# Performance work log

Hardware: AMD Instinct MI355X
Metric: run time of the kernel (lower is better)

Reference implementation:

```python
import jax, jax.numpy as jnp
import numpy as np

EPSILON = 1e-05


def _sq_dist(x, e):
    # x: [N, D], e: [M, D] -> [N, M] squared euclidean distances (addmm form)
    return (jnp.sum(e ** 2, axis=1)[None, :]
            + jnp.sum(x ** 2, axis=1, keepdims=True)
            - 2.0 * (x @ e.T))


def _mode_along_last(idx, M):
    # idx: [B, T] int32 -> [B] mode (smallest value among most frequent, like torch.mode)
    def one(row):
        counts = jnp.zeros((M,), dtype=jnp.int32).at[row].add(1)
        return jnp.argmax(counts)
    return jax.vmap(one)(idx)


def setup_inputs() -> dict:
    key = jax.random.key(0)
    k1, k2, k3 = jax.random.split(key, 3)
    B, T, D, M = 64, 512, 512, 1024
    audio_semantic = jax.random.normal(k1, (B, T, D), dtype=jnp.float32)
    video_semantic = jax.random.normal(k2, (B, T, D), dtype=jnp.float32)
    init_bound = 1.0 / M
    embedding = jax.random.uniform(k3, (M, 2 * D), dtype=jnp.float32,
                                   minval=-init_bound, maxval=init_bound)
    log_ratio = float(np.log(0.8 / 0.2))
    modality_weights = jnp.zeros((M, 4), dtype=jnp.float32)
    modality_weights = modality_weights.at[:, 0].set(log_ratio).at[:, 3].set(log_ratio)
    return {"audio_semantic": audio_semantic, "video_semantic": video_semantic,
            "embedding": embedding, "modality_weights": modality_weights, "epoch": 1}


def reference(audio_semantic, video_semantic, embedding, modality_weights, epoch):
    M, D_total = embedding.shape
    B, T, D = audio_semantic.shape
    video_embedding = embedding[:, :D]   # [M, D]
    audio_embedding = embedding[:, D:]   # [M, D]

    a_flat = audio_semantic.reshape(-1, D)  # [B*T, D]
    v_flat = video_semantic.reshape(-1, D)

    v_distances = _sq_dist(v_flat, video_embedding)  # [B*T, M]
    a_distances = _sq_dist(a_flat, audio_embedding)

    # cross-modal matching probabilities (clamp for sqrt numerical safety)
    v_ph = jax.nn.softmax(-jnp.sqrt(jnp.maximum(v_distances, 0.0)), axis=1)
    a_ph = jax.nn.softmax(-jnp.sqrt(jnp.maximum(a_distances, 0.0)), axis=1)
    v_pH = jnp.mean(v_ph.reshape(B, T, M), axis=1)  # [B, M]
    a_pH = jnp.mean(a_ph.reshape(B, T, M), axis=1)

    Scode = a_pH @ jnp.log(v_pH.T + 1e-10) + v_pH @ jnp.log(a_pH.T + 1e-10)  # [B, B]
    MaxScode = jnp.max(-Scode)
    EScode = jnp.exp(Scode + MaxScode)
    EScode_sumdim1 = jnp.sum(EScode, axis=1)
    Lcmcm_av = -jnp.mean(jnp.log(jnp.diag(EScode) / (EScode_sumdim1 + EPSILON)))

    v_indices = jnp.argmin(v_distances, axis=-1)  # [B*T]
    a_indices = jnp.argmin(a_distances, axis=-1)

    # straight-through quantization
    v_q = video_embedding[v_indices].reshape(B, T, D)
    a_q = audio_embedding[a_indices].reshape(B, T, D)
    v_quantized = video_semantic + jax.lax.stop_gradient(v_q - video_semantic)
    a_quantized = audio_semantic + jax.lax.stop_gradient(a_q - audio_semantic)

    v_full_vectors = embedding[v_indices].reshape(B, T, D_total)
    a_full_vectors = embedding[a_indices].reshape(B, T, D_total)

    v_mode = _mode_along_last(v_indices.reshape(B, T), M)
    a_mode = _mode_along_last(a_indices.reshape(B, T), M)
    equal_num = jnp.sum(v_mode == a_mode)

    return (v_full_vectors, a_full_vectors, v_quantized, a_quantized, Lcmcm_av, equal_num)
```

## Files before the change

### kernel.cpp

```cpp
#include <hip/hip_runtime.h>
#include <stdint.h>

typedef unsigned long long u64;

#define NROWS 32768
#define DK    512
#define MM    1024

#define WS_ET    0u
#define WS_SE    4194304u
#define WS_PH    4202496u
#define WS_CNT   4726784u
#define WS_IDX   5251072u
#define WS_SC    5513216u
#define WS_MODES 5529600u

__global__ void k_se(const float* __restrict__ E, float* __restrict__ se) {
  int t = threadIdx.x;
  int row = blockIdx.x * 4 + (t >> 6);
  int lane = t & 63;
  int mod = row >> 10, m = row & 1023;
  const float4* er = (const float4*)(E + (size_t)m * 1024 + mod * 512);
  float4 a = er[lane * 2], b = er[lane * 2 + 1];
  float s = a.x*a.x + a.y*a.y + a.z*a.z + a.w*a.w
          + b.x*b.x + b.y*b.y + b.z*b.z + b.w*b.w;
  #pragma unroll
  for (int o = 1; o < 64; o <<= 1) s += __shfl_xor(s, o, 64);
  if (lane == 0) se[row] = s;
}

__global__ void k_transpose(const float* __restrict__ E, float* __restrict__ Et) {
  __shared__ float tile[32][33];
  int t = threadIdx.x;
  int kt = blockIdx.x & 15, mt = blockIdx.x >> 4, mod = blockIdx.y;
  int j = t & 31, i0 = t >> 5;
  for (int ii = i0; ii < 32; ii += 8)
    tile[ii][j] = E[(size_t)(mt*32 + ii) * 1024 + mod*512 + kt*32 + j];
  __syncthreads();
  int mm2 = t & 31, kx = t >> 5;
  for (int kk = kx; kk < 32; kk += 8)
    Et[(size_t)mod * 524288 + (size_t)(kt*32 + kk) * 1024 + mt*32 + mm2] = tile[mm2][kk];
}

__global__ __launch_bounds__(256, 2) void k_main(
    const float* __restrict__ vsem, const float* __restrict__ asem,
    const float* __restrict__ Et, const float* __restrict__ se,
    float* __restrict__ pH, int* __restrict__ cnt, int* __restrict__ idx)
{
  __shared__ float Bs[16][1024];
  __shared__ __align__(16) float As[16][36];
  __shared__ float pH_part[1024];
  __shared__ float sx_lds[32];

  const int t = threadIdx.x;
  const int mod = blockIdx.y;
  const int r0 = blockIdx.x * 32;
  const int rg = t >> 6, cg = t & 63;
  const float* x = mod ? asem : vsem;

  {
    int r = t >> 4, kl = t & 15;
    #pragma unroll
    for (int h = 0; h < 2; ++h) {
      const float* xr = x + (size_t)(r0 + r + h * 16) * DK;
      float s = 0.f;
      for (int k = kl; k < DK; k += 16) { float v = xr[k]; s = fmaf(v, v, s); }
      #pragma unroll
      for (int o = 1; o < 16; o <<= 1) s += __shfl_xor(s, o, 64);
      if (kl == 0) sx_lds[r + h * 16] = s;
    }
  }

  float acc[128];
  #pragma unroll
  for (int q = 0; q < 128; ++q) acc[q] = 0.f;

  for (int k0 = 0; k0 < DK; k0 += 16) {
    __syncthreads();
    {
      int akl = t & 15, ar = t >> 4;
      As[akl][ar]      = x[(size_t)(r0 + ar) * DK + k0 + akl];
      As[akl][ar + 16] = x[(size_t)(r0 + ar + 16) * DK + k0 + akl];
    }
    #pragma unroll
    for (int kk = 0; kk < 16; ++kk)
      *(float4*)&Bs[kk][t * 4] =
          ((const float4*)(Et + (size_t)mod * 524288 + (size_t)(k0 + kk) * 1024))[t];
    __syncthreads();
    #pragma unroll
    for (int kk = 0; kk < 16; ++kk) {
      const float4 a0 = *(const float4*)&As[kk][rg * 8];
      const float4 a1 = *(const float4*)&As[kk][rg * 8 + 4];
      const float4 b0 = *(const float4*)&Bs[kk][cg * 4];
      const float4 b1 = *(const float4*)&Bs[kk][256 + cg * 4];
      const float4 b2 = *(const float4*)&Bs[kk][512 + cg * 4];
      const float4 b3 = *(const float4*)&Bs[kk][768 + cg * 4];
      #pragma unroll
      for (int rr = 0; rr < 8; ++rr) {
        const float av = rr == 0 ? a0.x : rr == 1 ? a0.y : rr == 2 ? a0.z :
                         rr == 3 ? a0.w : rr == 4 ? a1.x : rr == 5 ? a1.y :
                         rr == 6 ? a1.z : a1.w;
        float* ar = acc + rr * 16;
        ar[0] = fmaf(av, b0.x, ar[0]);  ar[1] = fmaf(av, b0.y, ar[1]);
        ar[2] = fmaf(av, b0.z, ar[2]);  ar[3] = fmaf(av, b0.w, ar[3]);
        ar[4] = fmaf(av, b1.x, ar[4]);  ar[5] = fmaf(av, b1.y, ar[5]);
        ar[6] = fmaf(av, b1.z, ar[6]);  ar[7] = fmaf(av, b1.w, ar[7]);
        ar[8] = fmaf(av, b2.x, ar[8]);  ar[9] = fmaf(av, b2.y, ar[9]);
        ar[10] = fmaf(av, b2.z, ar[10]); ar[11] = fmaf(av, b2.w, ar[11]);
        ar[12] = fmaf(av, b3.x, ar[12]); ar[13] = fmaf(av, b3.y, ar[13]);
        ar[14] = fmaf(av, b3.z, ar[14]); ar[15] = fmaf(av, b3.w, ar[15]);
      }
    }
  }

  float sxv[8];
  #pragma unroll
  for (int rr = 0; rr < 8; ++rr) sxv[rr] = sx_lds[rg * 8 + rr];
  const float* seB = se + mod * 1024;

  float rowsum[8] = {0.f, 0.f, 0.f, 0.f, 0.f, 0.f, 0.f, 0.f};
  u64 bk[8] = {~0ull, ~0ull, ~0ull, ~0ull, ~0ull, ~0ull, ~0ull, ~0ull};
  #pragma unroll
  for (int j = 0; j < 4; ++j)
    #pragma unroll
    for (int i = 0; i < 4; ++i) {
      const int m = j * 256 + cg * 4 + i;
      const float sem = seB[m];
      #pragma unroll
      for (int rr = 0; rr < 8; ++rr) {
        const float d = (sem + sxv[rr]) - 2.0f * acc[rr * 16 + j * 4 + i];
        const float s = sqrtf(fmaxf(d, 0.0f));
        const float ww = __expf(-s);
        acc[rr * 16 + j * 4 + i] = ww;
        rowsum[rr] += ww;
        unsigned ub = __float_as_uint(d);
        ub = (ub & 0x80000000u) ? ~ub : (ub | 0x80000000u);
        u64 key = ((u64)ub << 32) | (u64)(unsigned)m;
        bk[rr] = key < bk[rr] ? key : bk[rr];
      }
    }
  #pragma unroll
  for (int o = 1; o < 64; o <<= 1) {
    #pragma unroll
    for (int rr = 0; rr < 8; ++rr) {
      rowsum[rr] += __shfl_xor(rowsum[rr], o, 64);
      u64 ok = __shfl_xor(bk[rr], o, 64);
      bk[rr] = ok < bk[rr] ? ok : bk[rr];
    }
  }

  const int b = r0 >> 9;
  if (cg == 0) {
    #pragma unroll
    for (int rr = 0; rr < 8; ++rr) {
      const int row = r0 + rg * 8 + rr;
      const int m = (int)(bk[rr] & 0xFFFFFFFFull);
      idx[mod * NROWS + row] = m;
      atomicAdd(&cnt[((mod * 64 + b) << 10) + m], 1);
    }
  }

  float inv[8];
  #pragma unroll
  for (int rr = 0; rr < 8; ++rr) inv[rr] = 1.0f / rowsum[rr];

  for (int q = t; q < 1024; q += 256) pH_part[q] = 0.f;
  __syncthreads();
  #pragma unroll
  for (int j = 0; j < 4; ++j)
    #pragma unroll
    for (int i = 0; i < 4; ++i) {
      const int m = j * 256 + cg * 4 + i;
      float v = 0.f;
      #pragma unroll
      for (int rr = 0; rr < 8; ++rr) v += acc[rr * 16 + j * 4 + i] * inv[rr];
      atomicAdd(&pH_part[m], v);
    }
  __syncthreads();
  for (int q = t; q < 1024; q += 256)
    atomicAdd(&pH[((mod * 64 + b) << 10) + q], pH_part[q] * (1.0f / 512.0f));
}

__global__ void k_modes(const int* __restrict__ cnt, int* __restrict__ modes) {
  __shared__ u64 red[4];
  int t = threadIdx.x;
  int mod = blockIdx.x >> 6, b = blockIdx.x & 63;
  const int* c = cnt + ((mod * 64 + b) << 10);
  u64 best = 0;
  for (int m = t; m < 1024; m += 256) {
    u64 key = ((u64)(unsigned)c[m] << 32) | (u64)(0xFFFFFFFFu - (unsigned)m);
    best = key > best ? key : best;
  }
  #pragma unroll
  for (int o = 1; o < 64; o <<= 1) { u64 ok = __shfl_xor(best, o, 64); best = ok > best ? ok : best; }
  if ((t & 63) == 0) red[t >> 6] = best;
  __syncthreads();
  if (t == 0) {
    #pragma unroll
    for (int q = 1; q < 4; ++q) best = red[q] > best ? red[q] : best;
    modes[mod * 64 + b] = (int)(0xFFFFFFFFu - (unsigned)(best & 0xFFFFFFFFull));
  }
}

__global__ void k_equal(const int* __restrict__ modes, float* __restrict__ out5) {
  int t = threadIdx.x;
  float e = (modes[t] == modes[64 + t]) ? 1.0f : 0.0f;
  #pragma unroll
  for (int o = 1; o < 64; o <<= 1) e += __shfl_xor(e, o, 64);
  if (t == 0) out5[0] = e;
}

__global__ void k_scode(const float* __restrict__ pH, float* __restrict__ Sc) {
  int t = threadIdx.x;
  int i = blockIdx.x;
  int j = t >> 2, part = t & 3;
  const float* vH = pH;
  const float* aH = pH + 65536;
  const float* ai = aH + i * 1024;
  const float* vi = vH + i * 1024;
  const float* vj = vH + j * 1024;
  const float* aj = aH + j * 1024;
  float s = 0.f;
  for (int m = part * 256; m < part * 256 + 256; ++m)
    s += ai[m] * logf(vj[m] + 1e-10f) + vi[m] * logf(aj[m] + 1e-10f);
  s += __shfl_xor(s, 1, 64);
  s += __shfl_xor(s, 2, 64);
  if (part == 0) Sc[i * 64 + j] = s;
}

__global__ void k_lcmcm(const float* __restrict__ Sc, float* __restrict__ out4) {
  __shared__ float red[4];
  __shared__ float maxs_sh;
  int t = threadIdx.x;
  float mx = -3.402823466e38f;
  for (int q = t; q < 4096; q += 256) mx = fmaxf(mx, -Sc[q]);
  #pragma unroll
  for (int o = 1; o < 64; o <<= 1) mx = fmaxf(mx, __shfl_xor(mx, o, 64));
  if ((t & 63) == 0) red[t >> 6] = mx;
  __syncthreads();
  if (t == 0) maxs_sh = fmaxf(fmaxf(red[0], red[1]), fmaxf(red[2], red[3]));
  __syncthreads();
  float maxS = maxs_sh;
  if (t < 64) {
    float sum = 0.f, diag = 0.f;
    for (int j2 = 0; j2 < 64; ++j2) {
      float e = expf(Sc[t * 64 + j2] + maxS);
      sum += e;
      if (j2 == t) diag = e;
    }
    float li = logf(diag / (sum + 1e-5f));
    #pragma unroll
    for (int o = 1; o < 64; o <<= 1) li += __shfl_xor(li, o, 64);
    if (t == 0) out4[0] = -(li * (1.0f / 64.0f));
  }
}

__global__ __launch_bounds__(256) void k_gather(
    const float* __restrict__ E, const float* __restrict__ vsem,
    const float* __restrict__ asem, const int* __restrict__ idx,
    float* __restrict__ out0, float* __restrict__ out1,
    float* __restrict__ out2, float* __restrict__ out3)
{
  int n = blockIdx.x, t = threadIdx.x;
  int iv = idx[n], ia = idx[NROWS + n];
  const float4* E4 = (const float4*)E;
  ((float4*)(out0 + (size_t)n * 1024))[t] = E4[iv * 256 + t];
  ((float4*)(out1 + (size_t)n * 1024))[t] = E4[ia * 256 + t];
  if (t < 128) {
    float4 q = E4[iv * 256 + t];
    float4 xv = ((const float4*)(vsem + (size_t)n * 512))[t];
    float4 r;
    r.x = xv.x + (q.x - xv.x); r.y = xv.y + (q.y - xv.y);
    r.z = xv.z + (q.z - xv.z); r.w = xv.w + (q.w - xv.w);
    ((float4*)(out2 + (size_t)n * 512))[t] = r;
  } else {
    int u = t - 128;
    float4 q = E4[ia * 256 + 128 + u];
    float4 xa = ((const float4*)(asem + (size_t)n * 512))[u];
    float4 r;
    r.x = xa.x + (q.x - xa.x); r.y = xa.y + (q.y - xa.y);
    r.z = xa.z + (q.z - xa.z); r.w = xa.w + (q.w - xa.w);
    ((float4*)(out3 + (size_t)n * 512))[u] = r;
  }
}

extern "C" void kernel_launch(void* const* d_in, const int* in_sizes, int n_in,
                              void* d_out, int out_size, void* d_ws, size_t ws_size,
                              hipStream_t stream) {
  const float* asem = (const float*)d_in[0];
  const float* vsem = (const float*)d_in[1];
  const float* E    = (const float*)d_in[2];
  char* ws = (char*)d_ws;
  float* Et    = (float*)(ws + WS_ET);
  float* se    = (float*)(ws + WS_SE);
  float* pH    = (float*)(ws + WS_PH);
  int*   cnt   = (int*)(ws + WS_CNT);
  int*   idx   = (int*)(ws + WS_IDX);
  float* Sc    = (float*)(ws + WS_SC);
  int*   modes = (int*)(ws + WS_MODES);
  float* out = (float*)d_out;

  hipMemsetAsync(ws + WS_PH, 0, 1048576, stream);

  hipLaunchKernelGGL(k_se, dim3(512), dim3(256), 0, stream, E, se);
  hipLaunchKernelGGL(k_transpose, dim3(512, 2), dim3(256), 0, stream, E, Et);
  hipLaunchKernelGGL(k_main, dim3(1024, 2), dim3(256), 0, stream,
                     vsem, asem, Et, se, pH, cnt, idx);
  hipLaunchKernelGGL(k_modes, dim3(128), dim3(256), 0, stream, cnt, modes);
  hipLaunchKernelGGL(k_equal, dim3(1), dim3(64), 0, stream, modes,
                     out + 100663297ull);
  hipLaunchKernelGGL(k_scode, dim3(64), dim3(256), 0, stream, pH, Sc);
  hipLaunchKernelGGL(k_lcmcm, dim3(1), dim3(256), 0, stream, Sc,
                     out + 100663296ull);
  hipLaunchKernelGGL(k_gather, dim3(32768), dim3(256), 0, stream,
                     E, vsem, asem, idx,
                     out, out + 33554432ull, out + 67108864ull, out + 83886080ull);
}
```

Baseline: 1.444 ms.

## Double-buffer codebook tiles via direct global-to-LDS loads in distance GEMM

The main distance kernel now uses 512-thread blocks covering 64 rows. Codebook tiles are double-buffered in LDS and filled with async global_load_lds so the next k-slice streams in while the current one is computed. The activation tile is no longer staged in LDS; each thread reads its rows straight from global memory as float4s. This halves the number of barriers per k-step and shares each codebook tile across twice as many rows, at the cost of uncoalesced per-thread activation loads and a larger LDS footprint (about 128KB for Bs alone).

```diff
diff --git a/kernel.cpp b/kernel.cpp
--- a/kernel.cpp
+++ b/kernel.cpp
@@ -15,6 +15,14 @@
 #define WS_SC    5513216u
 #define WS_MODES 5529600u
 
+__device__ __forceinline__ void gl_lds16(const float* g, float* l) {
+  auto* gp = reinterpret_cast<const __attribute__((address_space(1))) unsigned int*>(
+      reinterpret_cast<uintptr_t>(g));
+  auto* lp = reinterpret_cast<__attribute__((address_space(3))) unsigned int*>(
+      reinterpret_cast<uintptr_t>(l));
+  __builtin_amdgcn_global_load_lds(gp, lp, 16, 0, 0);
+}
+
 __global__ void k_se(const float* __restrict__ E, float* __restrict__ se) {
   int t = threadIdx.x;
   int row = blockIdx.x * 4 + (t >> 6);
@@ -42,32 +50,40 @@
     Et[(size_t)mod * 524288 + (size_t)(kt*32 + kk) * 1024 + mt*32 + mm2] = tile[mm2][kk];
 }
 
-__global__ __launch_bounds__(256, 2) void k_main(
+__global__ __launch_bounds__(512) __attribute__((amdgpu_waves_per_eu(2, 2)))
+void k_main(
     const float* __restrict__ vsem, const float* __restrict__ asem,
     const float* __restrict__ Et, const float* __restrict__ se,
     float* __restrict__ pH, int* __restrict__ cnt, int* __restrict__ idx)
 {
-  __shared__ float Bs[16][1024];
-  __shared__ __align__(16) float As[16][36];
+  __shared__ float Bs[2][16][1024];
   __shared__ float pH_part[1024];
-  __shared__ float sx_lds[32];
+  __shared__ float sx_lds[64];
 
   const int t = threadIdx.x;
   const int mod = blockIdx.y;
-  const int r0 = blockIdx.x * 32;
+  const int r0 = blockIdx.x * 64;
   const int rg = t >> 6, cg = t & 63;
   const float* x = mod ? asem : vsem;
+  const float* EtM = Et + (size_t)mod * 524288;
+
+  #pragma unroll
+  for (int i = 0; i < 8; ++i) {
+    const int q = rg * 8 + i;
+    gl_lds16(EtM + (q >> 2) * 1024 + (q & 3) * 256 + cg * 4,
+             &Bs[0][0][0] + q * 256);
+  }
 
   {
     int r = t >> 4, kl = t & 15;
     #pragma unroll
     for (int h = 0; h < 2; ++h) {
-      const float* xr = x + (size_t)(r0 + r + h * 16) * DK;
+      const float* xr = x + (size_t)(r0 + r + h * 32) * DK;
       float s = 0.f;
       for (int k = kl; k < DK; k += 16) { float v = xr[k]; s = fmaf(v, v, s); }
       #pragma unroll
       for (int o = 1; o < 16; o <<= 1) s += __shfl_xor(s, o, 64);
-      if (kl == 0) sx_lds[r + h * 16] = s;
+      if (kl == 0) sx_lds[r + h * 32] = s;
     }
   }
 
@@ -75,42 +91,50 @@
   #pragma unroll
   for (int q = 0; q < 128; ++q) acc[q] = 0.f;
 
+  __syncthreads();
+
+  int p = 0;
   for (int k0 = 0; k0 < DK; k0 += 16) {
+    if (k0 + 16 < DK) {
+      const float* Esrc = EtM + (size_t)(k0 + 16) * 1024;
+      #pragma unroll
+      for (int i = 0; i < 8; ++i) {
+        const int q = rg * 8 + i;
+        gl_lds16(Esrc + (q >> 2) * 1024 + (q & 3) * 256 + cg * 4,
+                 &Bs[p ^ 1][0][0] + q * 256);
+      }
+    }
+    #pragma unroll
+    for (int g = 0; g < 4; ++g) {
+      float4 xq[8];
+      #pragma unroll
+      for (int rr = 0; rr < 8; ++rr)
+        xq[rr] = *(const float4*)(x + (size_t)(r0 + rg * 8 + rr) * DK + k0 + g * 4);
+      #pragma unroll
+      for (int k2 = 0; k2 < 4; ++k2) {
+        const int kk = g * 4 + k2;
+        const float4 b0 = *(const float4*)&Bs[p][kk][cg * 4];
+        const float4 b1 = *(const float4*)&Bs[p][kk][256 + cg * 4];
+        const float4 b2 = *(const float4*)&Bs[p][kk][512 + cg * 4];
+        const float4 b3 = *(const float4*)&Bs[p][kk][768 + cg * 4];
+        #pragma unroll
+        for (int rr = 0; rr < 8; ++rr) {
+          const float av = k2 == 0 ? xq[rr].x : k2 == 1 ? xq[rr].y :
+                           k2 == 2 ? xq[rr].z : xq[rr].w;
+          float* ar = acc + rr * 16;
+          ar[0] = fmaf(av, b0.x, ar[0]);  ar[1] = fmaf(av, b0.y, ar[1]);
+          ar[2] = fmaf(av, b0.z, ar[2]);  ar[3] = fmaf(av, b0.w, ar[3]);
+          ar[4] = fmaf(av, b1.x, ar[4]);  ar[5] = fmaf(av, b1.y, ar[5]);
+          ar[6] = fmaf(av, b1.z, ar[6]);  ar[7] = fmaf(av, b1.w, ar[7]);
+          ar[8] = fmaf(av, b2.x, ar[8]);  ar[9] = fmaf(av, b2.y, ar[9]);
+          ar[10] = fmaf(av, b2.z, ar[10]); ar[11] = fmaf(av, b2.w, ar[11]);
+          ar[12] = fmaf(av, b3.x, ar[12]); ar[13] = fmaf(av, b3.y, ar[13]);
+          ar[14] = fmaf(av, b3.z, ar[14]); ar[15] = fmaf(av, b3.w, ar[15]);
+        }
+      }
+    }
     __syncthreads();
-    {
-      int akl = t & 15, ar = t >> 4;
-      As[akl][ar]      = x[(size_t)(r0 + ar) * DK + k0 + akl];
-      As[akl][ar + 16] = x[(size_t)(r0 + ar + 16) * DK + k0 + akl];
-    }
-    #pragma unroll
-    for (int kk = 0; kk < 16; ++kk)
-      *(float4*)&Bs[kk][t * 4] =
-          ((const float4*)(Et + (size_t)mod * 524288 + (size_t)(k0 + kk) * 1024))[t];
-    __syncthreads();
-    #pragma unroll
-    for (int kk = 0; kk < 16; ++kk) {
-      const float4 a0 = *(const float4*)&As[kk][rg * 8];
-      const float4 a1 = *(const float4*)&As[kk][rg * 8 + 4];
-      const float4 b0 = *(const float4*)&Bs[kk][cg * 4];
-      const float4 b1 = *(const float4*)&Bs[kk][256 + cg * 4];
-      const float4 b2 = *(const float4*)&Bs[kk][512 + cg * 4];
-      const float4 b3 = *(const float4*)&Bs[kk][768 + cg * 4];
-      #pragma unroll
-      for (int rr = 0; rr < 8; ++rr) {
-        const float av = rr == 0 ? a0.x : rr == 1 ? a0.y : rr == 2 ? a0.z :
-                         rr == 3 ? a0.w : rr == 4 ? a1.x : rr == 5 ? a1.y :
-                         rr == 6 ? a1.z : a1.w;
-        float* ar = acc + rr * 16;
-        ar[0] = fmaf(av, b0.x, ar[0]);  ar[1] = fmaf(av, b0.y, ar[1]);
-        ar[2] = fmaf(av, b0.z, ar[2]);  ar[3] = fmaf(av, b0.w, ar[3]);
-        ar[4] = fmaf(av, b1.x, ar[4]);  ar[5] = fmaf(av, b1.y, ar[5]);
-        ar[6] = fmaf(av, b1.z, ar[6]);  ar[7] = fmaf(av, b1.w, ar[7]);
-        ar[8] = fmaf(av, b2.x, ar[8]);  ar[9] = fmaf(av, b2.y, ar[9]);
-        ar[10] = fmaf(av, b2.z, ar[10]); ar[11] = fmaf(av, b2.w, ar[11]);
-        ar[12] = fmaf(av, b3.x, ar[12]); ar[13] = fmaf(av, b3.y, ar[13]);
-        ar[14] = fmaf(av, b3.z, ar[14]); ar[15] = fmaf(av, b3.w, ar[15]);
-      }
-    }
+    p ^= 1;
   }
 
   float sxv[8];
@@ -164,7 +188,7 @@
   #pragma unroll
   for (int rr = 0; rr < 8; ++rr) inv[rr] = 1.0f / rowsum[rr];
 
-  for (int q = t; q < 1024; q += 256) pH_part[q] = 0.f;
+  for (int q = t; q < 1024; q += 512) pH_part[q] = 0.f;
   __syncthreads();
   #pragma unroll
   for (int j = 0; j < 4; ++j)
@@ -177,7 +201,7 @@
       atomicAdd(&pH_part[m], v);
     }
   __syncthreads();
-  for (int q = t; q < 1024; q += 256)
+  for (int q = t; q < 1024; q += 512)
     atomicAdd(&pH[((mod * 64 + b) << 10) + q], pH_part[q] * (1.0f / 512.0f));
 }
 
@@ -304,7 +328,7 @@
 
   hipLaunchKernelGGL(k_se, dim3(512), dim3(256), 0, stream, E, se);
   hipLaunchKernelGGL(k_transpose, dim3(512, 2), dim3(256), 0, stream, E, Et);
-  hipLaunchKernelGGL(k_main, dim3(1024, 2), dim3(256), 0, stream,
+  hipLaunchKernelGGL(k_main, dim3(512, 2), dim3(512), 0, stream,
                      vsem, asem, Et, se, pH, cnt, idx);
   hipLaunchKernelGGL(k_modes, dim3(128), dim3(256), 0, stream, cnt, modes);
   hipLaunchKernelGGL(k_equal, dim3(1), dim3(64), 0, stream, modes,
```

Result: slower. 3.651 ms (+152.9%).
